# Performance work log

Measured on AMD Instinct MI355X. Metric: run time of the kernel, lower is better.

The kernel has to match this reference:

```python
import jax, jax.numpy as jnp
import numpy as np

# Typical Deformable-DETR pyramid for an 800x1200 image, strides 8/16/32/64
SPATIAL = np.array([[100, 150], [50, 75], [25, 38], [13, 19]], dtype=np.int64)


def setup_inputs() -> dict:
    key = jax.random.key(0)
    k1, k2, k3 = jax.random.split(key, 3)
    bs, heads, d, L, P = 2, 8, 32, 4, 4
    num_keys = int((SPATIAL[:, 0] * SPATIAL[:, 1]).sum())  # 18947
    Q = num_keys  # encoder self-attention: one query per key
    value = jax.random.normal(k1, (bs, num_keys, heads, d), dtype=jnp.float32)
    # normalized sampling coords in [0,1] (module maps to [-1,1] via 2*x-1)
    sampling_locations = jax.random.uniform(k2, (bs, Q, heads, L, P, 2), dtype=jnp.float32)
    w = jax.random.uniform(k3, (bs, Q, heads, L, P), dtype=jnp.float32)
    attention_weights = jax.nn.softmax(w.reshape(bs, Q, heads, L * P), axis=-1).reshape(bs, Q, heads, L, P)
    return {
        "value": value,
        "value_spatial_shapes": jnp.asarray(SPATIAL),
        "sampling_locations": sampling_locations,
        "attention_weights": attention_weights,
    }


def _bilinear_sample(v, grid):
    """F.grid_sample(mode='bilinear', padding_mode='zeros', align_corners=False).
    v: (N, H, W, d); grid: (N, Q, P, 2) with (x, y) in [-1, 1].
    Returns (N, Q, P, d)."""
    N, H, W, d = v.shape
    x = (grid[..., 0] + 1.0) * (W * 0.5) - 0.5
    y = (grid[..., 1] + 1.0) * (H * 0.5) - 0.5
    x0 = jnp.floor(x).astype(jnp.int32)
    y0 = jnp.floor(y).astype(jnp.int32)
    x1, y1 = x0 + 1, y0 + 1
    wx1 = x - x0
    wy1 = y - y0
    wx0 = 1.0 - wx1
    wy0 = 1.0 - wy1
    nidx = jnp.arange(N)[:, None, None]

    def gather(yy, xx):
        m = ((xx >= 0) & (xx < W) & (yy >= 0) & (yy < H)).astype(v.dtype)
        out = v[nidx, jnp.clip(yy, 0, H - 1), jnp.clip(xx, 0, W - 1)]  # (N,Q,P,d)
        return out * m[..., None]

    return (gather(y0, x0) * (wy0 * wx0)[..., None]
            + gather(y0, x1) * (wy0 * wx1)[..., None]
            + gather(y1, x0) * (wy1 * wx0)[..., None]
            + gather(y1, x1) * (wy1 * wx1)[..., None])


def reference(value, value_spatial_shapes, sampling_locations, attention_weights):
    shapes = np.asarray(value_spatial_shapes)  # static level shapes
    bs, num_keys, heads, d = value.shape
    _, Q, _, L, P, _ = sampling_locations.shape
    grids = 2.0 * sampling_locations - 1.0  # (bs,Q,heads,L,P,2)
    sampled = []
    start = 0
    for lvl in range(L):
        H, W = int(shapes[lvl, 0]), int(shapes[lvl, 1])
        v = value[:, start:start + H * W]  # (bs, H*W, heads, d)
        start += H * W
        v = v.transpose(0, 2, 1, 3).reshape(bs * heads, H, W, d)
        g = grids[:, :, :, lvl].transpose(0, 2, 1, 3, 4).reshape(bs * heads, Q, P, 2)
        sampled.append(_bilinear_sample(v, g))  # (bs*heads, Q, P, d)
    s = jnp.stack(sampled, axis=2)  # (bs*heads, Q, L, P, d)
    w = attention_weights.transpose(0, 2, 1, 3, 4).reshape(bs * heads, Q, L, P)
    out = jnp.einsum('nqlpd,nqlp->nqd', s, w)  # (bs*heads, Q, d)
    # feature layout matches torch: channel index = head*d + c
    return out.reshape(bs, heads, Q, d).transpose(0, 2, 1, 3).reshape(bs, Q, heads * d)
```

## Files before the change

kernel.cpp:

```cpp
#include <hip/hip_runtime.h>
#include <hip/hip_fp16.h>


#define KQ 19947
#define NBQ (2 * KQ)

__global__ __launch_bounds__(256) void transpose_f16(
    const float* __restrict__ V, __half* __restrict__ Vh)
{
    const int pair = blockIdx.y;
    const int j = blockIdx.x * 256 + threadIdx.x;
    if (j >= KQ * 4) return;
    const int k = j >> 2, cg = j & 3;
    const int b = pair >> 3, h = pair & 7;
    const float* src = V + (((size_t)b * KQ + k) * 8 + h) * 32 + cg * 8;
    const float4 a0 = *reinterpret_cast<const float4*>(src);
    const float4 a1 = *reinterpret_cast<const float4*>(src + 4);
    __half2 h0 = __floats2half2_rn(a0.x, a0.y);
    __half2 h1 = __floats2half2_rn(a0.z, a0.w);
    __half2 h2 = __floats2half2_rn(a1.x, a1.y);
    __half2 h3 = __floats2half2_rn(a1.z, a1.w);
    uint4 o;
    o.x = *reinterpret_cast<unsigned int*>(&h0);
    o.y = *reinterpret_cast<unsigned int*>(&h1);
    o.z = *reinterpret_cast<unsigned int*>(&h2);
    o.w = *reinterpret_cast<unsigned int*>(&h3);
    reinterpret_cast<uint4*>(Vh + ((size_t)pair * KQ) * 32)[j] = o;
}

__global__ __launch_bounds__(256, 4) void msda_fwd_t(
    const __half* __restrict__ Vh,
    const float* __restrict__ LOC,
    const float* __restrict__ W,
    float* __restrict__ OUT)
{
    const int pair = blockIdx.x & 15;
    const int qc   = blockIdx.x >> 4;
    const int tid  = threadIdx.x;
    const int s    = tid & 7;
    const int slot = s >> 2;
    const float slotf = (float)slot;
    const int q    = qc * 32 + (tid >> 3);
    if (q >= KQ) return;
    const int b = pair >> 3, h = pair & 7;

    const int Hs[4]  = {100, 50, 25, 13};
    const int Ws[4]  = {150, 75, 38, 19};
    const int STs[4] = {0, 15000, 18750, 19700};

    const __half* vbl = Vh + (size_t)pair * KQ * 32 + s * 8;
    const float* lp = LOC + (((size_t)b * KQ + q) * 8 + h) * 32;
    const float* wp = W   + (((size_t)b * KQ + q) * 8 + h) * 16;

    float acc[8];
    #pragma unroll
    for (int c = 0; c < 8; ++c) acc[c] = 0.f;

    #pragma unroll
    for (int l = 0; l < 4; ++l) {
        const int Hh = Hs[l], Ww = Ws[l], st = STs[l];
        const float Hf = (float)Hh, Wf = (float)Ww;
        const float4 w4 = *reinterpret_cast<const float4*>(wp + l * 4);
        const float4 g0 = *reinterpret_cast<const float4*>(lp + l * 8);
        const float4 g1 = *reinterpret_cast<const float4*>(lp + l * 8 + 4);
        const float lx[4] = {g0.x, g0.z, g1.x, g1.z};
        const float ly[4] = {g0.y, g0.w, g1.y, g1.w};
        const float ww[4] = {w4.x, w4.y, w4.z, w4.w};

        int   off[8];
        float cw[8];
        #pragma unroll
        for (int p = 0; p < 4; ++p) {
            const float x = fmaf(lx[p], Wf, -0.5f);
            const float y = fmaf(ly[p], Hf, -0.5f);
            const float fy = floorf(y);
            const int y0 = (int)fy;
            const int x0 = (int)floorf(x);
            const int bx = min(max(x0, 0), Ww - 2);
            const float wxl = fmaxf(0.f, 1.f - fabsf(x - ((float)bx + slotf)));
            const float wy1 = y - fy, wy0 = 1.f - wy1;
            const int y0c = max(y0, 0);
            const int y1c = min(y0 + 1, Hh - 1);
            const float ay0 = (y0 >= 0)     ? wy0 : 0.f;
            const float ay1 = (y0 + 1 < Hh) ? wy1 : 0.f;
            const float wl = ww[p] * wxl;
            off[2*p]   = (st + y0c * Ww + bx) << 5;
            off[2*p+1] = (st + y1c * Ww + bx) << 5;
            cw[2*p]    = wl * ay0;
            cw[2*p+1]  = wl * ay1;
        }

        uint4 v[8];
        #pragma unroll
        for (int i = 0; i < 8; ++i)
            v[i] = *reinterpret_cast<const uint4*>(vbl + off[i]);

        __half2 accH[4];
        #pragma unroll
        for (int j = 0; j < 4; ++j) accH[j] = __half2(__half(0.f), __half(0.f));

        #pragma unroll
        for (int i = 0; i < 8; ++i) {
            const __half2 wh = __floats2half2_rn(cw[i], cw[i]);
            union { uint4 u; __half2 h2[4]; } uv;
            uv.u = v[i];
            #pragma unroll
            for (int j = 0; j < 4; ++j)
                accH[j] = __hfma2(wh, uv.h2[j], accH[j]);
        }
        #pragma unroll
        for (int j = 0; j < 4; ++j) {
            const float2 f = __half22float2(accH[j]);
            acc[2*j]   += f.x;
            acc[2*j+1] += f.y;
        }
    }

    #pragma unroll
    for (int c = 0; c < 8; ++c)
        acc[c] += __shfl_xor(acc[c], 4, 64);

    float* op = OUT + ((size_t)b * KQ + q) * 256 + h * 32 + (s & 3) * 8 + slot * 4;
    *reinterpret_cast<float4*>(op) =
        make_float4(acc[slot*4], acc[slot*4+1], acc[slot*4+2], acc[slot*4+3]);
}

static __device__ __forceinline__ void fmadd4(float4& a, float s, const float4 v) {
    a.x = fmaf(s, v.x, a.x);
    a.y = fmaf(s, v.y, a.y);
    a.z = fmaf(s, v.z, a.z);
    a.w = fmaf(s, v.w, a.w);
}

__global__ __launch_bounds__(256, 4) void msda_fwd_f32(
    const float* __restrict__ V,
    const float* __restrict__ LOC,
    const float* __restrict__ W,
    float* __restrict__ OUT)
{
    const int t  = blockIdx.x * 256 + threadIdx.x;
    const int cg = t & 7;
    const int h  = (t >> 3) & 7;
    const int bq = t >> 6;
    if (bq >= NBQ) return;
    const int b = (bq >= KQ) ? 1 : 0;

    const int Hs[4]  = {100, 50, 25, 13};
    const int Ws[4]  = {150, 75, 38, 19};
    const int STs[4] = {0, 15000, 18750, 19700};

    const int hoff = (h << 5) + (cg << 2);
    const float* vb = V + (size_t)b * KQ * 256 + hoff;
    const float* lp = LOC + ((size_t)bq * 8 + h) * 32;
    const float* wp = W   + ((size_t)bq * 8 + h) * 16;

    float4 acc = make_float4(0.f, 0.f, 0.f, 0.f);

    #pragma unroll
    for (int l = 0; l < 4; ++l) {
        const int Hh = Hs[l], Ww = Ws[l], st = STs[l];
        const float Hf = (float)Hh, Wf = (float)Ww;
        const float4 w4 = *reinterpret_cast<const float4*>(wp + l * 4);
        const float4 g0 = *reinterpret_cast<const float4*>(lp + l * 8);
        const float4 g1 = *reinterpret_cast<const float4*>(lp + l * 8 + 4);
        const float lx[4] = {g0.x, g0.z, g1.x, g1.z};
        const float ly[4] = {g0.y, g0.w, g1.y, g1.w};
        const float ww[4] = {w4.x, w4.y, w4.z, w4.w};
        #pragma unroll
        for (int p = 0; p < 4; ++p) {
            const float x = fmaf(lx[p], Wf, -0.5f);
            const float y = fmaf(ly[p], Hf, -0.5f);
            const float fx = floorf(x), fy = floorf(y);
            const int x0 = (int)fx, y0 = (int)fy;
            const float wx1 = x - fx, wy1 = y - fy;
            const float wx0 = 1.f - wx1, wy0 = 1.f - wy1;
            const int x0c = max(x0, 0),     x1c = min(x0 + 1, Ww - 1);
            const int y0c = max(y0, 0),     y1c = min(y0 + 1, Hh - 1);
            const float ax0 = (x0 >= 0)      ? wx0 : 0.f;
            const float ax1 = (x0 + 1 < Ww)  ? wx1 : 0.f;
            const float ay0 = (y0 >= 0)      ? wy0 : 0.f;
            const float ay1 = (y0 + 1 < Hh)  ? wy1 : 0.f;
            const float w = ww[p];
            const int b0 = st + y0c * Ww, b1 = st + y1c * Ww;
            fmadd4(acc, w*ay0*ax0, *reinterpret_cast<const float4*>(vb + ((b0+x0c) << 8)));
            fmadd4(acc, w*ay0*ax1, *reinterpret_cast<const float4*>(vb + ((b0+x1c) << 8)));
            fmadd4(acc, w*ay1*ax0, *reinterpret_cast<const float4*>(vb + ((b1+x0c) << 8)));
            fmadd4(acc, w*ay1*ax1, *reinterpret_cast<const float4*>(vb + ((b1+x1c) << 8)));
        }
    }
    *reinterpret_cast<float4*>(OUT + (size_t)bq * 256 + hoff) = acc;
}

extern "C" void kernel_launch(void* const* d_in, const int* in_sizes, int n_in,
                              void* d_out, int out_size, void* d_ws, size_t ws_size,
                              hipStream_t stream) {
    const float* V   = (const float*)d_in[0];
    const float* LOC = (const float*)d_in[2];
    const float* W   = (const float*)d_in[3];
    float* OUT = (float*)d_out;

    const size_t n_val = (size_t)2 * KQ * 256;
    const size_t need  = n_val * sizeof(__half) + 256;

    if (ws_size >= need) {
        __half* Vh = (__half*)d_ws;
        const int jtot = KQ * 4;
        dim3 tgrid((jtot + 255) / 256, 16);
        hipLaunchKernelGGL(transpose_f16, tgrid, dim3(256), 0, stream, V, Vh);

        const int qchunks = (KQ + 31) / 32;
        const int blocks  = qchunks * 16;
        hipLaunchKernelGGL(msda_fwd_t, dim3(blocks), dim3(256), 0, stream,
                           Vh, LOC, W, OUT);
    } else {
        const int total = NBQ * 64;
        hipLaunchKernelGGL(msda_fwd_f32, dim3((total + 255) / 256), dim3(256), 0, stream,
                           V, LOC, W, OUT);
    }
}
```

Baseline: 96.35 us.

## Software-pipeline level gathers with double-buffered loads in fp16 sampling kernel

Restructures the per-level loop into an explicit two-stage software pipeline, so the gathers for the next level are issued before the current level's fp16 FMAs. This is meant to overlap gather latency with address math and compute. It adds template-specialised level constants and lowers the launch-bounds occupancy hint from 4 to 3 to make room for the extra register buffers. Fewer resident waves could reduce latency hiding in return.

```diff
diff --git a/kernel.cpp b/kernel.cpp
--- a/kernel.cpp
+++ b/kernel.cpp
@@ -28,7 +28,79 @@
     reinterpret_cast<uint4*>(Vh + ((size_t)pair * KQ) * 32)[j] = o;
 }
 
-__global__ __launch_bounds__(256, 4) void msda_fwd_t(
+__constant__ int c_Hs[4]  = {100, 50, 25, 13};
+__constant__ int c_Ws[4]  = {150, 75, 38, 19};
+__constant__ int c_STs[4] = {0, 15000, 18750, 19700};
+
+template<int L>
+static __device__ __forceinline__ void addr_level(
+    const float* __restrict__ lp, const float* __restrict__ wp,
+    float slotf, int off[8], float cw[8])
+{
+    constexpr int Hh = (L == 0) ? 100 : (L == 1) ? 50 : (L == 2) ? 25 : 13;
+    constexpr int Ww = (L == 0) ? 150 : (L == 1) ? 75 : (L == 2) ? 38 : 19;
+    constexpr int st = (L == 0) ? 0 : (L == 1) ? 15000 : (L == 2) ? 18750 : 19700;
+    const float Hf = (float)Hh, Wf = (float)Ww;
+    const float4 w4 = *reinterpret_cast<const float4*>(wp + L * 4);
+    const float4 g0 = *reinterpret_cast<const float4*>(lp + L * 8);
+    const float4 g1 = *reinterpret_cast<const float4*>(lp + L * 8 + 4);
+    const float lx[4] = {g0.x, g0.z, g1.x, g1.z};
+    const float ly[4] = {g0.y, g0.w, g1.y, g1.w};
+    const float ww[4] = {w4.x, w4.y, w4.z, w4.w};
+    #pragma unroll
+    for (int p = 0; p < 4; ++p) {
+        const float x = fmaf(lx[p], Wf, -0.5f);
+        const float y = fmaf(ly[p], Hf, -0.5f);
+        const float fy = floorf(y);
+        const int y0 = (int)fy;
+        const int x0 = (int)floorf(x);
+        const int bx = min(max(x0, 0), Ww - 2);
+        const float wxl = fmaxf(0.f, 1.f - fabsf(x - ((float)bx + slotf)));
+        const float wy1 = y - fy, wy0 = 1.f - wy1;
+        const int y0c = max(y0, 0);
+        const int y1c = min(y0 + 1, Hh - 1);
+        const float ay0 = (y0 >= 0)     ? wy0 : 0.f;
+        const float ay1 = (y0 + 1 < Hh) ? wy1 : 0.f;
+        const float wl = ww[p] * wxl;
+        off[2*p]   = (st + y0c * Ww + bx) << 5;
+        off[2*p+1] = (st + y1c * Ww + bx) << 5;
+        cw[2*p]    = wl * ay0;
+        cw[2*p+1]  = wl * ay1;
+    }
+}
+
+static __device__ __forceinline__ void load_level(
+    const __half* __restrict__ vbl, const int off[8], uint4 v[8])
+{
+    #pragma unroll
+    for (int i = 0; i < 8; ++i)
+        v[i] = *reinterpret_cast<const uint4*>(vbl + off[i]);
+}
+
+static __device__ __forceinline__ void consume_level(
+    const uint4 v[8], const float cw[8], float acc[8])
+{
+    __half2 accH[4];
+    #pragma unroll
+    for (int j = 0; j < 4; ++j) accH[j] = __half2(__half(0.f), __half(0.f));
+    #pragma unroll
+    for (int i = 0; i < 8; ++i) {
+        const __half2 wh = __floats2half2_rn(cw[i], cw[i]);
+        union { uint4 u; __half2 h2[4]; } uv;
+        uv.u = v[i];
+        #pragma unroll
+        for (int j = 0; j < 4; ++j)
+            accH[j] = __hfma2(wh, uv.h2[j], accH[j]);
+    }
+    #pragma unroll
+    for (int j = 0; j < 4; ++j) {
+        const float2 f = __half22float2(accH[j]);
+        acc[2*j]   += f.x;
+        acc[2*j+1] += f.y;
+    }
+}
+
+__global__ __launch_bounds__(256, 3) void msda_fwd_t(
     const __half* __restrict__ Vh,
     const float* __restrict__ LOC,
     const float* __restrict__ W,
@@ -44,10 +116,6 @@
     if (q >= KQ) return;
     const int b = pair >> 3, h = pair & 7;
 
-    const int Hs[4]  = {100, 50, 25, 13};
-    const int Ws[4]  = {150, 75, 38, 19};
-    const int STs[4] = {0, 15000, 18750, 19700};
-
     const __half* vbl = Vh + (size_t)pair * KQ * 32 + s * 8;
     const float* lp = LOC + (((size_t)b * KQ + q) * 8 + h) * 32;
     const float* wp = W   + (((size_t)b * KQ + q) * 8 + h) * 16;
@@ -56,65 +124,25 @@
     #pragma unroll
     for (int c = 0; c < 8; ++c) acc[c] = 0.f;
 
-    #pragma unroll
-    for (int l = 0; l < 4; ++l) {
-        const int Hh = Hs[l], Ww = Ws[l], st = STs[l];
-        const float Hf = (float)Hh, Wf = (float)Ww;
-        const float4 w4 = *reinterpret_cast<const float4*>(wp + l * 4);
-        const float4 g0 = *reinterpret_cast<const float4*>(lp + l * 8);
-        const float4 g1 = *reinterpret_cast<const float4*>(lp + l * 8 + 4);
-        const float lx[4] = {g0.x, g0.z, g1.x, g1.z};
-        const float ly[4] = {g0.y, g0.w, g1.y, g1.w};
-        const float ww[4] = {w4.x, w4.y, w4.z, w4.w};
-
-        int   off[8];
-        float cw[8];
-        #pragma unroll
-        for (int p = 0; p < 4; ++p) {
-            const float x = fmaf(lx[p], Wf, -0.5f);
-            const float y = fmaf(ly[p], Hf, -0.5f);
-            const float fy = floorf(y);
-            const int y0 = (int)fy;
-            const int x0 = (int)floorf(x);
-            const int bx = min(max(x0, 0), Ww - 2);
-            const float wxl = fmaxf(0.f, 1.f - fabsf(x - ((float)bx + slotf)));
-            const float wy1 = y - fy, wy0 = 1.f - wy1;
-            const int y0c = max(y0, 0);
-            const int y1c = min(y0 + 1, Hh - 1);
-            const float ay0 = (y0 >= 0)     ? wy0 : 0.f;
-            const float ay1 = (y0 + 1 < Hh) ? wy1 : 0.f;
-            const float wl = ww[p] * wxl;
-            off[2*p]   = (st + y0c * Ww + bx) << 5;
-            off[2*p+1] = (st + y1c * Ww + bx) << 5;
-            cw[2*p]    = wl * ay0;
-            cw[2*p+1]  = wl * ay1;
-        }
-
-        uint4 v[8];
-        #pragma unroll
-        for (int i = 0; i < 8; ++i)
-            v[i] = *reinterpret_cast<const uint4*>(vbl + off[i]);
-
-        __half2 accH[4];
-        #pragma unroll
-        for (int j = 0; j < 4; ++j) accH[j] = __half2(__half(0.f), __half(0.f));
-
-        #pragma unroll
-        for (int i = 0; i < 8; ++i) {
-            const __half2 wh = __floats2half2_rn(cw[i], cw[i]);
-            union { uint4 u; __half2 h2[4]; } uv;
-            uv.u = v[i];
-            #pragma unroll
-            for (int j = 0; j < 4; ++j)
-                accH[j] = __hfma2(wh, uv.h2[j], accH[j]);
-        }
-        #pragma unroll
-        for (int j = 0; j < 4; ++j) {
-            const float2 f = __half22float2(accH[j]);
-            acc[2*j]   += f.x;
-            acc[2*j+1] += f.y;
-        }
-    }
+    int off0[8], off1[8];
+    float cw0[8], cw1[8];
+    uint4 va[8], vb2[8];
+
+    addr_level<0>(lp, wp, slotf, off0, cw0);
+    load_level(vbl, off0, va);
+    addr_level<1>(lp, wp, slotf, off1, cw1);
+    load_level(vbl, off1, vb2);
+
+    consume_level(va, cw0, acc);
+    addr_level<2>(lp, wp, slotf, off0, cw0);
+    load_level(vbl, off0, va);
+
+    consume_level(vb2, cw1, acc);
+    addr_level<3>(lp, wp, slotf, off1, cw1);
+    load_level(vbl, off1, vb2);
+
+    consume_level(va, cw0, acc);
+    consume_level(vb2, cw1, acc);
 
     #pragma unroll
     for (int c = 0; c < 8; ++c)
```

After: 95.99 us. About the same (-0.4%).
